# Performance work log

Measured on AMD Instinct MI355X. Metric: run time of the kernel, lower is better.

Reference implementation:

```python
import jax, jax.numpy as jnp
import numpy as np

N_NODES = 100000
BN_EPS = 1e-5


def gcn_conv(x, W, b, src, dst, n_nodes):
    # PyG GCNConv: linear transform, add self loops, symmetric deg^-1/2 normalization, sum-aggregate to dst, add bias
    h = x @ W.T  # [N, out_dim]
    loops = jnp.arange(n_nodes, dtype=src.dtype)
    src_a = jnp.concatenate([src, loops])
    dst_a = jnp.concatenate([dst, loops])
    deg = jnp.zeros((n_nodes,), dtype=h.dtype).at[dst_a].add(1.0)  # includes self loops, so deg >= 1
    dinv = jax.lax.rsqrt(deg)
    norm = dinv[src_a] * dinv[dst_a]  # [E+N]
    msgs = h[src_a] * norm[:, None]  # gather + scale
    out = jax.ops.segment_sum(msgs, dst_a, num_segments=n_nodes)
    return out + b


def batch_norm(x, gamma, beta):
    # BatchNorm1d in training mode: per-feature batch mean/var (biased)
    mean = jnp.mean(x, axis=0)
    var = jnp.var(x, axis=0)
    return (x - mean) * jax.lax.rsqrt(var + BN_EPS) * gamma + beta


def setup_inputs() -> dict:
    key = jax.random.key(0)
    ks = jax.random.split(key, 8)
    n, e = N_NODES, 1600000
    d_in, d_hid, d_out = 128, 128, 64
    x = jax.random.normal(ks[0], (n, d_in), dtype=jnp.float32)
    edge_index = jax.random.randint(ks[1], (2, e), 0, n, dtype=jnp.int64)
    W1 = jax.random.normal(ks[2], (d_hid, d_in), dtype=jnp.float32) / np.sqrt(d_in)
    b1 = jnp.zeros((d_hid,), dtype=jnp.float32)
    gamma = jnp.ones((d_hid,), dtype=jnp.float32)
    beta = jnp.zeros((d_hid,), dtype=jnp.float32)
    W2 = jax.random.normal(ks[3], (d_out, d_hid), dtype=jnp.float32) / np.sqrt(d_hid)
    b2 = jnp.zeros((d_out,), dtype=jnp.float32)
    return {"x": x, "edge_index": edge_index, "W1": W1, "b1": b1,
            "gamma": gamma, "beta": beta, "W2": W2, "b2": b2}


def reference(x, edge_index, W1, b1, gamma, beta, W2, b2):
    src, dst = edge_index[0], edge_index[1]
    n = x.shape[0]
    h = gcn_conv(x, W1, b1, src, dst, n)          # layer 0 conv
    h = batch_norm(h, gamma, beta)                 # BN
    h = jax.nn.relu(h)                             # ReLU (dropout p=0 -> identity)
    out = gcn_conv(h, W2, b2, src, dst, n)         # layer 1 conv (no BN/act on last layer)
    return out
```

## Files before the change

### kernel.cpp

```cpp
#include <hip/hip_runtime.h>

constexpr float BN_EPS = 1e-5f;
#define BSH 7
#define NBMAX 1024

typedef __attribute__((ext_vector_type(8))) short bf16x8;
typedef __attribute__((ext_vector_type(4))) float f32x4;

__device__ inline float2 bf2x2(unsigned int v) {
    union { unsigned int i; float f; } a, b;
    a.i = v << 16;
    b.i = v & 0xFFFF0000u;
    return make_float2(a.f, b.f);
}
__device__ inline float bf2f(unsigned short u) {
    union { unsigned int i; float f; } a;
    a.i = ((unsigned int)u) << 16;
    return a.f;
}
__device__ inline unsigned short f2bf(float f) {
    union { float f; unsigned int i; } c;
    c.f = f;
    unsigned int i = c.i;
    return (unsigned short)((i + 0x7FFFu + ((i >> 16) & 1u)) >> 16);
}

__device__ inline int wsw(int row, int k) {
    return row * 128 + ((((k >> 3) ^ (row & 7)) << 3) | (k & 7));
}

__global__ void k_zero(int* __restrict__ gcount) {
    gcount[threadIdx.x] = 0;
}

__global__ __launch_bounds__(256) void k_hist(const int* __restrict__ dst, int* __restrict__ gcount,
                                              int E, int NB) {
    __shared__ int lh[NBMAX];
    const int tid = threadIdx.x;
    for (int i = tid; i < NBMAX; i += 256) lh[i] = 0;
    __syncthreads();
    const int base = blockIdx.x * 8192;
#pragma unroll
    for (int i = 0; i < 32; ++i) {
        int e = base + i * 256 + tid;
        if (e < E) atomicAdd(&lh[dst[e] >> BSH], 1);
    }
    __syncthreads();
    for (int b = tid; b < NB; b += 256) {
        int c = lh[b];
        if (c) atomicAdd(&gcount[b], c);
    }
}

__global__ __launch_bounds__(1024) void k_scanb(const int* __restrict__ gcount, int* __restrict__ gstart,
                                                int* __restrict__ cursor, float* __restrict__ stats, int NB) {
    __shared__ int tmp[1024];
    const int t = threadIdx.x;
    int v = (t < NB) ? gcount[t] : 0;
    tmp[t] = v;
    __syncthreads();
    for (int off = 1; off < 1024; off <<= 1) {
        int u = (t >= off) ? tmp[t - off] : 0;
        __syncthreads();
        tmp[t] += u;
        __syncthreads();
    }
    if (t < NB) { int ex = tmp[t] - v; gstart[t] = ex; cursor[t] = ex; }
    if (t == NB - 1) gstart[NB] = tmp[t];
    if (t < 512) stats[t] = 0.f;
}

__global__ __launch_bounds__(256) void k_scatter(const int* __restrict__ src, const int* __restrict__ dst,
                                                 int* __restrict__ cursor, int2* __restrict__ pairs,
                                                 int E, int NB) {
    __shared__ int lh[NBMAX], lbase[NBMAX], gbase[NBMAX], lcur[NBMAX];
    __shared__ int2 buf[4096];
    __shared__ unsigned short bo[4096];
    const int tid = threadIdx.x;
    for (int i = tid; i < NBMAX; i += 256) lh[i] = 0;
    __syncthreads();
    const int base = blockIdx.x * 4096;
    const int cnt = min(4096, E - base);
#pragma unroll
    for (int i = 0; i < 16; ++i) {
        int e = base + i * 256 + tid;
        if (e < E) atomicAdd(&lh[dst[e] >> BSH], 1);
    }
    __syncthreads();
    int s0 = lh[tid * 4], s1 = lh[tid * 4 + 1], s2 = lh[tid * 4 + 2], s3 = lh[tid * 4 + 3];
    int ts = s0 + s1 + s2 + s3;
    lcur[tid] = ts;
    __syncthreads();
    for (int off = 1; off < 256; off <<= 1) {
        int u = (tid >= off) ? lcur[tid - off] : 0;
        __syncthreads();
        lcur[tid] += u;
        __syncthreads();
    }
    int ex = lcur[tid] - ts;
    lbase[tid * 4] = ex;
    lbase[tid * 4 + 1] = ex + s0;
    lbase[tid * 4 + 2] = ex + s0 + s1;
    lbase[tid * 4 + 3] = ex + s0 + s1 + s2;
    __syncthreads();
    for (int b = tid; b < NB; b += 256) {
        int c = lh[b];
        gbase[b] = c ? atomicAdd(&cursor[b], c) : 0;
    }
    for (int i = tid; i < NBMAX; i += 256) lcur[i] = 0;
    __syncthreads();
#pragma unroll
    for (int i = 0; i < 16; ++i) {
        int e = base + i * 256 + tid;
        if (e < E) {
            int d = dst[e];
            int b = d >> BSH;
            int p = lbase[b] + atomicAdd(&lcur[b], 1);
            buf[p] = make_int2(src[e], d);
            bo[p] = (unsigned short)b;
        }
    }
    __syncthreads();
#pragma unroll
    for (int i = 0; i < 16; ++i) {
        int p = i * 256 + tid;
        if (p < cnt) {
            int b = bo[p];
            pairs[gbase[b] + (p - lbase[b])] = buf[p];
        }
    }
}

__global__ __launch_bounds__(256) void k_build(const int2* __restrict__ pairs, const int* __restrict__ gstart,
                                               int* __restrict__ rowptr, int* __restrict__ rowend,
                                               float* __restrict__ dinv, int* __restrict__ esrc, int n) {
    __shared__ int lh[128], lsc[128], lcur[128];
    const int tid = threadIdx.x;
    const int b = blockIdx.x;
    const int e0 = gstart[b], e1 = gstart[b + 1];
    const int node0 = b << BSH;
    if (tid < 128) lh[tid] = 0;
    __syncthreads();
    for (int e = e0 + tid; e < e1; e += 256) atomicAdd(&lh[pairs[e].y - node0], 1);
    __syncthreads();
    int v = (tid < 128) ? lh[tid] : 0;
    if (tid < 128) lsc[tid] = v;
    __syncthreads();
    for (int off = 1; off < 128; off <<= 1) {
        int u = (tid >= off && tid < 128) ? lsc[tid - off] : 0;
        __syncthreads();
        if (tid < 128) lsc[tid] += u;
        __syncthreads();
    }
    if (tid < 128) {
        int ex = lsc[tid] - v;
        lcur[tid] = ex;
        int node = node0 + tid;
        if (node < n) {
            int rp = e0 + ex;
            rowptr[node] = rp;
            rowend[node] = rp + v;
            dinv[node] = rsqrtf((float)(v + 1));
        }
    }
    __syncthreads();
    for (int e = e0 + tid; e < e1; e += 256) {
        int2 p = pairs[e];
        int pos = atomicAdd(&lcur[p.y - node0], 1);
        esrc[e0 + pos] = p.x;
    }
}

__global__ __launch_bounds__(256) void k_gemm1(const float* __restrict__ x,
                                               const float* __restrict__ W1,
                                               const float* __restrict__ dinv,
                                               unsigned short* __restrict__ g1, int n) {
    __shared__ unsigned short Ws[128 * 128];
    const int tid = threadIdx.x;
#pragma unroll
    for (int i = 0; i < 16; ++i) {
        int idx4 = i * 256 + tid;
        int j = idx4 >> 5;
        int k = (idx4 & 31) * 4;
        float4 v = *(const float4*)&W1[(size_t)j * 128 + k];
        ushort4 u;
        u.x = f2bf(v.x); u.y = f2bf(v.y); u.z = f2bf(v.z); u.w = f2bf(v.w);
        *(ushort2*)&Ws[wsw(j, k)] = make_ushort2(u.x, u.y);
        *(ushort2*)&Ws[wsw(j, k + 2)] = make_ushort2(u.z, u.w);
    }
    __syncthreads();
    const int wave = tid >> 6, l = tid & 63;
    const int am = l & 15;
    const int kg = l >> 4;
    const int row0 = blockIdx.x * 64 + wave * 16;
    const int grow = row0 + am;
    const float* xrow = &x[(size_t)(grow < n ? grow : 0) * 128];
    f32x4 acc[8] = {};
#pragma unroll
    for (int k0 = 0; k0 < 128; k0 += 32) {
        const int kk = k0 + kg * 8;
        float4 a0 = *(const float4*)&xrow[kk];
        float4 a1 = *(const float4*)&xrow[kk + 4];
        union { unsigned short u[8]; bf16x8 v; } af;
        af.u[0] = f2bf(a0.x); af.u[1] = f2bf(a0.y); af.u[2] = f2bf(a0.z); af.u[3] = f2bf(a0.w);
        af.u[4] = f2bf(a1.x); af.u[5] = f2bf(a1.y); af.u[6] = f2bf(a1.z); af.u[7] = f2bf(a1.w);
#pragma unroll
        for (int ct = 0; ct < 8; ++ct) {
            union { uint4 q; bf16x8 v; } bf;
            bf.q = *(const uint4*)&Ws[wsw(ct * 16 + am, kk)];
            acc[ct] = __builtin_amdgcn_mfma_f32_16x16x32_bf16(af.v, bf.v, acc[ct], 0, 0, 0);
        }
    }
#pragma unroll
    for (int r = 0; r < 4; ++r) {
        int orow = row0 + kg * 4 + r;
        if (orow < n) {
            float di = dinv[orow];
#pragma unroll
            for (int ct = 0; ct < 8; ++ct)
                g1[(size_t)orow * 128 + ct * 16 + am] = f2bf(acc[ct][r] * di);
        }
    }
}

__global__ __launch_bounds__(256) void k_pull1(const int* __restrict__ rowptr, const int* __restrict__ rowend,
                                               const int* __restrict__ esrc, const unsigned short* __restrict__ g,
                                               const float* __restrict__ dinv, const float* __restrict__ b1,
                                               unsigned short* __restrict__ h1, float* __restrict__ stats, int n) {
    __shared__ float2 sSum[4][64];
    __shared__ float2 sSq[4][64];
    const int wid = threadIdx.x >> 6, lane = threadIdx.x & 63;
    const int gw = blockIdx.x * 4 + wid;
    const int nw = gridDim.x * 4;
    const float2 bias = *(const float2*)&b1[lane * 2];
    float2 psum = {0.f, 0.f}, psq = {0.f, 0.f};
    for (int node = gw; node < n; node += nw) {
        const int b = rowptr[node], e = rowend[node];
        float2 a0 = bf2x2(*(const unsigned int*)&g[(size_t)node * 128 + lane * 2]);
        float2 a1 = {0.f, 0.f}, a2 = {0.f, 0.f}, a3 = {0.f, 0.f};
        float2 a4 = {0.f, 0.f}, a5 = {0.f, 0.f}, a6 = {0.f, 0.f}, a7 = {0.f, 0.f};
        int j = b;
        for (; j + 8 <= e; j += 8) {
            int s0 = esrc[j + 0], s1 = esrc[j + 1], s2 = esrc[j + 2], s3 = esrc[j + 3];
            int s4 = esrc[j + 4], s5 = esrc[j + 5], s6 = esrc[j + 6], s7 = esrc[j + 7];
            unsigned int v0 = *(const unsigned int*)&g[(size_t)s0 * 128 + lane * 2];
            unsigned int v1 = *(const unsigned int*)&g[(size_t)s1 * 128 + lane * 2];
            unsigned int v2 = *(const unsigned int*)&g[(size_t)s2 * 128 + lane * 2];
            unsigned int v3 = *(const unsigned int*)&g[(size_t)s3 * 128 + lane * 2];
            unsigned int v4 = *(const unsigned int*)&g[(size_t)s4 * 128 + lane * 2];
            unsigned int v5 = *(const unsigned int*)&g[(size_t)s5 * 128 + lane * 2];
            unsigned int v6 = *(const unsigned int*)&g[(size_t)s6 * 128 + lane * 2];
            unsigned int v7 = *(const unsigned int*)&g[(size_t)s7 * 128 + lane * 2];
            float2 f0 = bf2x2(v0), f1 = bf2x2(v1), f2 = bf2x2(v2), f3 = bf2x2(v3);
            float2 f4 = bf2x2(v4), f5 = bf2x2(v5), f6 = bf2x2(v6), f7 = bf2x2(v7);
            a0.x += f0.x; a0.y += f0.y;
            a1.x += f1.x; a1.y += f1.y;
            a2.x += f2.x; a2.y += f2.y;
            a3.x += f3.x; a3.y += f3.y;
            a4.x += f4.x; a4.y += f4.y;
            a5.x += f5.x; a5.y += f5.y;
            a6.x += f6.x; a6.y += f6.y;
            a7.x += f7.x; a7.y += f7.y;
        }
        for (; j < e; ++j) {
            int s = esrc[j];
            float2 v = bf2x2(*(const unsigned int*)&g[(size_t)s * 128 + lane * 2]);
            a0.x += v.x; a0.y += v.y;
        }
        float2 acc = {((a0.x + a1.x) + (a2.x + a3.x)) + ((a4.x + a5.x) + (a6.x + a7.x)),
                      ((a0.y + a1.y) + (a2.y + a3.y)) + ((a4.y + a5.y) + (a6.y + a7.y))};
        const float di = dinv[node];
        float2 hv = {fmaf(acc.x, di, bias.x), fmaf(acc.y, di, bias.y)};
        unsigned int pk = ((unsigned int)f2bf(hv.y) << 16) | (unsigned int)f2bf(hv.x);
        *(unsigned int*)&h1[(size_t)node * 128 + lane * 2] = pk;
        psum.x += hv.x; psum.y += hv.y;
        psq.x = fmaf(hv.x, hv.x, psq.x);
        psq.y = fmaf(hv.y, hv.y, psq.y);
    }
    sSum[wid][lane] = psum;
    sSq[wid][lane] = psq;
    __syncthreads();
    if (threadIdx.x < 64) {
        float2 a = sSum[0][lane], b = sSum[1][lane], c = sSum[2][lane], d = sSum[3][lane];
        atomicAdd(&stats[lane * 2 + 0], a.x + b.x + c.x + d.x);
        atomicAdd(&stats[lane * 2 + 1], a.y + b.y + c.y + d.y);
        a = sSq[0][lane]; b = sSq[1][lane]; c = sSq[2][lane]; d = sSq[3][lane];
        atomicAdd(&stats[128 + lane * 2 + 0], a.x + b.x + c.x + d.x);
        atomicAdd(&stats[128 + lane * 2 + 1], a.y + b.y + c.y + d.y);
    }
}

__global__ void k_bnfinal(float* __restrict__ stats, const float* __restrict__ gamma,
                          const float* __restrict__ beta, int n) {
    int f = threadIdx.x;
    float inv_n = 1.f / (float)n;
    float mean = stats[f] * inv_n;
    float var = stats[128 + f] * inv_n - mean * mean;
    float sc = gamma[f] * rsqrtf(var + BN_EPS);
    stats[256 + f] = sc;
    stats[384 + f] = fmaf(-mean, sc, beta[f]);
}

__global__ __launch_bounds__(256) void k_gemm2(const unsigned short* __restrict__ h1,
                                               const float* __restrict__ W2,
                                               const float* __restrict__ dinv,
                                               const float* __restrict__ stats,
                                               unsigned short* __restrict__ g2, int n) {
    __shared__ unsigned short Ws[64 * 128];
    const int tid = threadIdx.x;
#pragma unroll
    for (int i = 0; i < 8; ++i) {
        int idx4 = i * 256 + tid;
        int j = idx4 >> 5;
        int k = (idx4 & 31) * 4;
        float4 v = *(const float4*)&W2[(size_t)j * 128 + k];
        ushort4 u;
        u.x = f2bf(v.x); u.y = f2bf(v.y); u.z = f2bf(v.z); u.w = f2bf(v.w);
        *(ushort2*)&Ws[wsw(j, k)] = make_ushort2(u.x, u.y);
        *(ushort2*)&Ws[wsw(j, k + 2)] = make_ushort2(u.z, u.w);
    }
    __syncthreads();
    const int wave = tid >> 6, l = tid & 63;
    const int am = l & 15;
    const int kg = l >> 4;
    const int row0 = blockIdx.x * 64 + wave * 16;
    const int grow = row0 + am;
    const unsigned short* hrow = &h1[(size_t)(grow < n ? grow : 0) * 128];
    f32x4 acc[4] = {};
#pragma unroll
    for (int k0 = 0; k0 < 128; k0 += 32) {
        const int kk = k0 + kg * 8;
        uint4 hq = *(const uint4*)&hrow[kk];
        float2 p0 = bf2x2(hq.x), p1 = bf2x2(hq.y), p2 = bf2x2(hq.z), p3 = bf2x2(hq.w);
        float hf[8] = {p0.x, p0.y, p1.x, p1.y, p2.x, p2.y, p3.x, p3.y};
        float4 sc0 = *(const float4*)&stats[256 + kk];
        float4 sc1 = *(const float4*)&stats[256 + kk + 4];
        float4 sh0 = *(const float4*)&stats[384 + kk];
        float4 sh1 = *(const float4*)&stats[384 + kk + 4];
        float scv[8] = {sc0.x, sc0.y, sc0.z, sc0.w, sc1.x, sc1.y, sc1.z, sc1.w};
        float shv[8] = {sh0.x, sh0.y, sh0.z, sh0.w, sh1.x, sh1.y, sh1.z, sh1.w};
        union { unsigned short u[8]; bf16x8 v; } af;
#pragma unroll
        for (int jj = 0; jj < 8; ++jj)
            af.u[jj] = f2bf(fmaxf(fmaf(hf[jj], scv[jj], shv[jj]), 0.f));
#pragma unroll
        for (int ct = 0; ct < 4; ++ct) {
            union { uint4 q; bf16x8 v; } bf;
            bf.q = *(const uint4*)&Ws[wsw(ct * 16 + am, kk)];
            acc[ct] = __builtin_amdgcn_mfma_f32_16x16x32_bf16(af.v, bf.v, acc[ct], 0, 0, 0);
        }
    }
#pragma unroll
    for (int r = 0; r < 4; ++r) {
        int orow = row0 + kg * 4 + r;
        if (orow < n) {
            float di = dinv[orow];
#pragma unroll
            for (int ct = 0; ct < 4; ++ct)
                g2[(size_t)orow * 64 + ct * 16 + am] = f2bf(acc[ct][r] * di);
        }
    }
}

__global__ __launch_bounds__(256) void k_pull2(const int* __restrict__ rowptr, const int* __restrict__ rowend,
                                               const int* __restrict__ esrc, const unsigned short* __restrict__ g,
                                               const float* __restrict__ dinv, const float* __restrict__ b2,
                                               float* __restrict__ out, int n) {
    const int wid = threadIdx.x >> 6, lane = threadIdx.x & 63;
    const int gw = blockIdx.x * 4 + wid;
    const int nw = gridDim.x * 4;
    const float bias = b2[lane];
    for (int node = gw; node < n; node += nw) {
        const int b = rowptr[node], e = rowend[node];
        float a0 = bf2f(g[(size_t)node * 64 + lane]);
        float a1 = 0.f, a2 = 0.f, a3 = 0.f, a4 = 0.f, a5 = 0.f, a6 = 0.f, a7 = 0.f;
        int j = b;
        for (; j + 8 <= e; j += 8) {
            int s0 = esrc[j + 0], s1 = esrc[j + 1], s2 = esrc[j + 2], s3 = esrc[j + 3];
            int s4 = esrc[j + 4], s5 = esrc[j + 5], s6 = esrc[j + 6], s7 = esrc[j + 7];
            unsigned short v0 = g[(size_t)s0 * 64 + lane];
            unsigned short v1 = g[(size_t)s1 * 64 + lane];
            unsigned short v2 = g[(size_t)s2 * 64 + lane];
            unsigned short v3 = g[(size_t)s3 * 64 + lane];
            unsigned short v4 = g[(size_t)s4 * 64 + lane];
            unsigned short v5 = g[(size_t)s5 * 64 + lane];
            unsigned short v6 = g[(size_t)s6 * 64 + lane];
            unsigned short v7 = g[(size_t)s7 * 64 + lane];
            a0 += bf2f(v0); a1 += bf2f(v1); a2 += bf2f(v2); a3 += bf2f(v3);
            a4 += bf2f(v4); a5 += bf2f(v5); a6 += bf2f(v6); a7 += bf2f(v7);
        }
        for (; j < e; ++j) a0 += bf2f(g[(size_t)esrc[j] * 64 + lane]);
        float acc = ((a0 + a1) + (a2 + a3)) + ((a4 + a5) + (a6 + a7));
        out[(size_t)node * 64 + lane] = fmaf(acc, dinv[node], bias);
    }
}

extern "C" void kernel_launch(void* const* d_in, const int* in_sizes, int n_in,
                              void* d_out, int out_size, void* d_ws, size_t ws_size,
                              hipStream_t stream) {
    const float* x     = (const float*)d_in[0];
    const int*   ei    = (const int*)d_in[1];
    const float* W1    = (const float*)d_in[2];
    const float* b1    = (const float*)d_in[3];
    const float* gamma = (const float*)d_in[4];
    const float* beta  = (const float*)d_in[5];
    const float* W2    = (const float*)d_in[6];
    const float* b2    = (const float*)d_in[7];
    float* out = (float*)d_out;

    const int n = in_sizes[0] / 128;
    const int E = in_sizes[1] / 2;
    const int* src = ei;
    const int* dst = ei + E;
    const int NB = (n + 127) >> BSH;
    const int Np = (n + 255) & ~255;
    const int Ep = (E + 3) & ~3;

    char* ws = (char*)d_ws;
    int*   gcount = (int*)ws;
    int*   gstart = gcount + 1024;
    int*   cursor = gstart + 1088;
    float* stats  = (float*)(cursor + 1024);
    float* dinv   = stats + 512;
    int*   rowptr = (int*)(dinv + Np);
    int*   rowend = rowptr + Np;
    int2*  pairs  = (int2*)(rowend + Np);
    int*   esrc   = (int*)(pairs + Ep);
    unsigned short* g1 = (unsigned short*)(esrc + Ep);
    unsigned short* h1 = g1 + (size_t)n * 128;
    unsigned short* g2 = g1;

    const int gb = (n + 63) / 64;
    const int gh = (E + 8191) / 8192;
    const int gs = (E + 4095) / 4096;

    hipLaunchKernelGGL(k_zero, dim3(1), dim3(1024), 0, stream, gcount);
    hipLaunchKernelGGL(k_hist, dim3(gh), dim3(256), 0, stream, dst, gcount, E, NB);
    hipLaunchKernelGGL(k_scanb, dim3(1), dim3(1024), 0, stream, gcount, gstart, cursor, stats, NB);
    hipLaunchKernelGGL(k_scatter, dim3(gs), dim3(256), 0, stream, src, dst, cursor, pairs, E, NB);
    hipLaunchKernelGGL(k_build, dim3(NB), dim3(256), 0, stream, pairs, gstart, rowptr, rowend, dinv, esrc, n);

    hipLaunchKernelGGL(k_gemm1, dim3(gb), dim3(256), 0, stream, x, W1, dinv, g1, n);
    hipLaunchKernelGGL(k_pull1, dim3(2048), dim3(256), 0, stream, rowptr, rowend, esrc, g1, dinv, b1, h1, stats, n);
    hipLaunchKernelGGL(k_bnfinal, dim3(1), dim3(128), 0, stream, stats, gamma, beta, n);

    hipLaunchKernelGGL(k_gemm2, dim3(gb), dim3(256), 0, stream, h1, W2, dinv, stats, g2, n);
    hipLaunchKernelGGL(k_pull2, dim3(2048), dim3(256), 0, stream, rowptr, rowend, esrc, g2, dinv, b2, out, n);
}
```

Measured before the change: 319.6 us.

## Split pull aggregation into feature slices with edge-parallel lanes per wave

Both pull kernels now give each block one feature slice (16 features in layer 1, 8 in layer 2), picked from the low bits of the block index. Each wave spreads its lanes across edges (8 or 16 edges in parallel) instead of across features, and the per-edge partial sums are combined with xor shuffles. The aim is more memory-level parallelism per node for the random gathers, and keeping each slice's working set smaller so it fits in cache better. In exchange, every node's neighbor list is read by 8 separate blocks, each gather moves only 32 or 16 bytes, and there is shuffle-reduction overhead; the kernel also now assumes the grid size is a multiple of 8.

Result: slower. 520.5 us (+62.8%).

```diff
diff --git a/kernel.cpp b/kernel.cpp
--- a/kernel.cpp
+++ b/kernel.cpp
@@ -227,66 +227,74 @@
                                                const int* __restrict__ esrc, const unsigned short* __restrict__ g,
                                                const float* __restrict__ dinv, const float* __restrict__ b1,
                                                unsigned short* __restrict__ h1, float* __restrict__ stats, int n) {
-    __shared__ float2 sSum[4][64];
-    __shared__ float2 sSq[4][64];
-    const int wid = threadIdx.x >> 6, lane = threadIdx.x & 63;
-    const int gw = blockIdx.x * 4 + wid;
-    const int nw = gridDim.x * 4;
-    const float2 bias = *(const float2*)&b1[lane * 2];
+    __shared__ float2 sS[4][8], sQ[4][8];
+    const int tid = threadIdx.x;
+    const int slice = blockIdx.x & 7;
+    const int wid = tid >> 6;
+    const int lane = tid & 63;
+    const int eslot = lane >> 3;
+    const int fl = lane & 7;
+    const int fbase = slice * 16 + fl * 2;
+    const int wv = (blockIdx.x >> 3) * 4 + wid;
+    const int nwv = (gridDim.x >> 3) * 4;
+    const float2 bias = *(const float2*)&b1[fbase];
     float2 psum = {0.f, 0.f}, psq = {0.f, 0.f};
-    for (int node = gw; node < n; node += nw) {
+    for (int node = wv; node < n; node += nwv) {
         const int b = rowptr[node], e = rowend[node];
-        float2 a0 = bf2x2(*(const unsigned int*)&g[(size_t)node * 128 + lane * 2]);
-        float2 a1 = {0.f, 0.f}, a2 = {0.f, 0.f}, a3 = {0.f, 0.f};
-        float2 a4 = {0.f, 0.f}, a5 = {0.f, 0.f}, a6 = {0.f, 0.f}, a7 = {0.f, 0.f};
+        float2 a0 = {0.f, 0.f}, a1 = {0.f, 0.f};
+        {
+            float2 s2 = bf2x2(*(const unsigned int*)&g[(size_t)node * 128 + fbase]);
+            if (eslot == 0) { a0.x += s2.x; a0.y += s2.y; }
+        }
         int j = b;
-        for (; j + 8 <= e; j += 8) {
-            int s0 = esrc[j + 0], s1 = esrc[j + 1], s2 = esrc[j + 2], s3 = esrc[j + 3];
-            int s4 = esrc[j + 4], s5 = esrc[j + 5], s6 = esrc[j + 6], s7 = esrc[j + 7];
-            unsigned int v0 = *(const unsigned int*)&g[(size_t)s0 * 128 + lane * 2];
-            unsigned int v1 = *(const unsigned int*)&g[(size_t)s1 * 128 + lane * 2];
-            unsigned int v2 = *(const unsigned int*)&g[(size_t)s2 * 128 + lane * 2];
-            unsigned int v3 = *(const unsigned int*)&g[(size_t)s3 * 128 + lane * 2];
-            unsigned int v4 = *(const unsigned int*)&g[(size_t)s4 * 128 + lane * 2];
-            unsigned int v5 = *(const unsigned int*)&g[(size_t)s5 * 128 + lane * 2];
-            unsigned int v6 = *(const unsigned int*)&g[(size_t)s6 * 128 + lane * 2];
-            unsigned int v7 = *(const unsigned int*)&g[(size_t)s7 * 128 + lane * 2];
-            float2 f0 = bf2x2(v0), f1 = bf2x2(v1), f2 = bf2x2(v2), f3 = bf2x2(v3);
-            float2 f4 = bf2x2(v4), f5 = bf2x2(v5), f6 = bf2x2(v6), f7 = bf2x2(v7);
+        for (; j + 16 <= e; j += 16) {
+            int s0 = esrc[j + eslot];
+            int s1 = esrc[j + 8 + eslot];
+            unsigned int v0 = *(const unsigned int*)&g[(size_t)s0 * 128 + fbase];
+            unsigned int v1 = *(const unsigned int*)&g[(size_t)s1 * 128 + fbase];
+            float2 f0 = bf2x2(v0), f1 = bf2x2(v1);
             a0.x += f0.x; a0.y += f0.y;
             a1.x += f1.x; a1.y += f1.y;
-            a2.x += f2.x; a2.y += f2.y;
-            a3.x += f3.x; a3.y += f3.y;
-            a4.x += f4.x; a4.y += f4.y;
-            a5.x += f5.x; a5.y += f5.y;
-            a6.x += f6.x; a6.y += f6.y;
-            a7.x += f7.x; a7.y += f7.y;
-        }
-        for (; j < e; ++j) {
-            int s = esrc[j];
-            float2 v = bf2x2(*(const unsigned int*)&g[(size_t)s * 128 + lane * 2]);
-            a0.x += v.x; a0.y += v.y;
-        }
-        float2 acc = {((a0.x + a1.x) + (a2.x + a3.x)) + ((a4.x + a5.x) + (a6.x + a7.x)),
-                      ((a0.y + a1.y) + (a2.y + a3.y)) + ((a4.y + a5.y) + (a6.y + a7.y))};
-        const float di = dinv[node];
-        float2 hv = {fmaf(acc.x, di, bias.x), fmaf(acc.y, di, bias.y)};
-        unsigned int pk = ((unsigned int)f2bf(hv.y) << 16) | (unsigned int)f2bf(hv.x);
-        *(unsigned int*)&h1[(size_t)node * 128 + lane * 2] = pk;
-        psum.x += hv.x; psum.y += hv.y;
-        psq.x = fmaf(hv.x, hv.x, psq.x);
-        psq.y = fmaf(hv.y, hv.y, psq.y);
-    }
-    sSum[wid][lane] = psum;
-    sSq[wid][lane] = psq;
-    __syncthreads();
-    if (threadIdx.x < 64) {
-        float2 a = sSum[0][lane], b = sSum[1][lane], c = sSum[2][lane], d = sSum[3][lane];
-        atomicAdd(&stats[lane * 2 + 0], a.x + b.x + c.x + d.x);
-        atomicAdd(&stats[lane * 2 + 1], a.y + b.y + c.y + d.y);
-        a = sSq[0][lane]; b = sSq[1][lane]; c = sSq[2][lane]; d = sSq[3][lane];
-        atomicAdd(&stats[128 + lane * 2 + 0], a.x + b.x + c.x + d.x);
-        atomicAdd(&stats[128 + lane * 2 + 1], a.y + b.y + c.y + d.y);
+        }
+        if (j < e) {
+            int i0 = j + eslot;
+            bool vv0 = i0 < e;
+            int s0 = vv0 ? esrc[i0] : node;
+            float2 f0 = bf2x2(*(const unsigned int*)&g[(size_t)s0 * 128 + fbase]);
+            if (vv0) { a0.x += f0.x; a0.y += f0.y; }
+            int i1 = j + 8 + eslot;
+            bool vv1 = i1 < e;
+            int s1 = vv1 ? esrc[i1] : node;
+            float2 f1 = bf2x2(*(const unsigned int*)&g[(size_t)s1 * 128 + fbase]);
+            if (vv1) { a1.x += f1.x; a1.y += f1.y; }
+        }
+        float2 acc = {a0.x + a1.x, a0.y + a1.y};
+        acc.x += __shfl_xor(acc.x, 8);  acc.y += __shfl_xor(acc.y, 8);
+        acc.x += __shfl_xor(acc.x, 16); acc.y += __shfl_xor(acc.y, 16);
+        acc.x += __shfl_xor(acc.x, 32); acc.y += __shfl_xor(acc.y, 32);
+        if (eslot == 0) {
+            const float di = dinv[node];
+            float2 hv = {fmaf(acc.x, di, bias.x), fmaf(acc.y, di, bias.y)};
+            unsigned int pk = ((unsigned int)f2bf(hv.y) << 16) | (unsigned int)f2bf(hv.x);
+            *(unsigned int*)&h1[(size_t)node * 128 + fbase] = pk;
+            psum.x += hv.x; psum.y += hv.y;
+            psq.x = fmaf(hv.x, hv.x, psq.x);
+            psq.y = fmaf(hv.y, hv.y, psq.y);
+        }
+    }
+    if (eslot == 0) { sS[wid][fl] = psum; sQ[wid][fl] = psq; }
+    __syncthreads();
+    if (tid < 8) {
+        float2 t = {0.f, 0.f}, q = {0.f, 0.f};
+#pragma unroll
+        for (int w = 0; w < 4; ++w) {
+            t.x += sS[w][tid].x; t.y += sS[w][tid].y;
+            q.x += sQ[w][tid].x; q.y += sQ[w][tid].y;
+        }
+        atomicAdd(&stats[slice * 16 + tid * 2 + 0], t.x);
+        atomicAdd(&stats[slice * 16 + tid * 2 + 1], t.y);
+        atomicAdd(&stats[128 + slice * 16 + tid * 2 + 0], q.x);
+        atomicAdd(&stats[128 + slice * 16 + tid * 2 + 1], q.y);
     }
 }
 
@@ -366,32 +374,55 @@
                                                const int* __restrict__ esrc, const unsigned short* __restrict__ g,
                                                const float* __restrict__ dinv, const float* __restrict__ b2,
                                                float* __restrict__ out, int n) {
-    const int wid = threadIdx.x >> 6, lane = threadIdx.x & 63;
-    const int gw = blockIdx.x * 4 + wid;
-    const int nw = gridDim.x * 4;
-    const float bias = b2[lane];
-    for (int node = gw; node < n; node += nw) {
+    const int tid = threadIdx.x;
+    const int slice = blockIdx.x & 7;
+    const int wid = tid >> 6;
+    const int lane = tid & 63;
+    const int eslot = lane >> 2;
+    const int fl = lane & 3;
+    const int fbase = slice * 8 + fl * 2;
+    const int wv = (blockIdx.x >> 3) * 4 + wid;
+    const int nwv = (gridDim.x >> 3) * 4;
+    const float2 bias = *(const float2*)&b2[fbase];
+    for (int node = wv; node < n; node += nwv) {
         const int b = rowptr[node], e = rowend[node];
-        float a0 = bf2f(g[(size_t)node * 64 + lane]);
-        float a1 = 0.f, a2 = 0.f, a3 = 0.f, a4 = 0.f, a5 = 0.f, a6 = 0.f, a7 = 0.f;
+        float2 a0 = {0.f, 0.f}, a1 = {0.f, 0.f};
+        {
+            float2 s2 = bf2x2(*(const unsigned int*)&g[(size_t)node * 64 + fbase]);
+            if (eslot == 0) { a0.x += s2.x; a0.y += s2.y; }
+        }
         int j = b;
-        for (; j + 8 <= e; j += 8) {
-            int s0 = esrc[j + 0], s1 = esrc[j + 1], s2 = esrc[j + 2], s3 = esrc[j + 3];
-            int s4 = esrc[j + 4], s5 = esrc[j + 5], s6 = esrc[j + 6], s7 = esrc[j + 7];
-            unsigned short v0 = g[(size_t)s0 * 64 + lane];
-            unsigned short v1 = g[(size_t)s1 * 64 + lane];
-            unsigned short v2 = g[(size_t)s2 * 64 + lane];
-            unsigned short v3 = g[(size_t)s3 * 64 + lane];
-            unsigned short v4 = g[(size_t)s4 * 64 + lane];
-            unsigned short v5 = g[(size_t)s5 * 64 + lane];
-            unsigned short v6 = g[(size_t)s6 * 64 + lane];
-            unsigned short v7 = g[(size_t)s7 * 64 + lane];
-            a0 += bf2f(v0); a1 += bf2f(v1); a2 += bf2f(v2); a3 += bf2f(v3);
-            a4 += bf2f(v4); a5 += bf2f(v5); a6 += bf2f(v6); a7 += bf2f(v7);
-        }
-        for (; j < e; ++j) a0 += bf2f(g[(size_t)esrc[j] * 64 + lane]);
-        float acc = ((a0 + a1) + (a2 + a3)) + ((a4 + a5) + (a6 + a7));
-        out[(size_t)node * 64 + lane] = fmaf(acc, dinv[node], bias);
+        for (; j + 32 <= e; j += 32) {
+            int s0 = esrc[j + eslot];
+            int s1 = esrc[j + 16 + eslot];
+            unsigned int v0 = *(const unsigned int*)&g[(size_t)s0 * 64 + fbase];
+            unsigned int v1 = *(const unsigned int*)&g[(size_t)s1 * 64 + fbase];
+            float2 f0 = bf2x2(v0), f1 = bf2x2(v1);
+            a0.x += f0.x; a0.y += f0.y;
+            a1.x += f1.x; a1.y += f1.y;
+        }
+        if (j < e) {
+            int i0 = j + eslot;
+            bool vv0 = i0 < e;
+            int s0 = vv0 ? esrc[i0] : node;
+            float2 f0 = bf2x2(*(const unsigned int*)&g[(size_t)s0 * 64 + fbase]);
+            if (vv0) { a0.x += f0.x; a0.y += f0.y; }
+            int i1 = j + 16 + eslot;
+            bool vv1 = i1 < e;
+            int s1 = vv1 ? esrc[i1] : node;
+            float2 f1 = bf2x2(*(const unsigned int*)&g[(size_t)s1 * 64 + fbase]);
+            if (vv1) { a1.x += f1.x; a1.y += f1.y; }
+        }
+        float2 acc = {a0.x + a1.x, a0.y + a1.y};
+        acc.x += __shfl_xor(acc.x, 4);  acc.y += __shfl_xor(acc.y, 4);
+        acc.x += __shfl_xor(acc.x, 8);  acc.y += __shfl_xor(acc.y, 8);
+        acc.x += __shfl_xor(acc.x, 16); acc.y += __shfl_xor(acc.y, 16);
+        acc.x += __shfl_xor(acc.x, 32); acc.y += __shfl_xor(acc.y, 32);
+        if (eslot == 0) {
+            const float di = dinv[node];
+            float2 o = {fmaf(acc.x, di, bias.x), fmaf(acc.y, di, bias.y)};
+            *(float2*)&out[(size_t)node * 64 + fbase] = o;
+        }
     }
 }
 
```
